# Kernel optimization log

Measured on AMD Instinct MI355X. Metric: run time of the kernel, lower is better.

The kernel has to match this reference:

```python
import jax, jax.numpy as jnp
import numpy as np

D_MSA = 256
D_PAIR = 128
N_HEADS = 8
HEAD_DIM = D_MSA // N_HEADS
EPS = 1e-5


def setup_inputs() -> dict:
    key = jax.random.key(0)
    ks = jax.random.split(key, 14)
    s = 0.02
    return {
        "msa": jax.random.normal(ks[0], (1, 64, 256, D_MSA), dtype=jnp.float32),
        "pair": jax.random.normal(ks[1], (1, 256, 256, D_PAIR), dtype=jnp.float32),
        "Wq": jax.random.normal(ks[2], (D_MSA, D_MSA), dtype=jnp.float32) * s,
        "bq": jnp.zeros((D_MSA,), jnp.float32),
        "Wk": jax.random.normal(ks[3], (D_MSA, D_MSA), dtype=jnp.float32) * s,
        "bk": jnp.zeros((D_MSA,), jnp.float32),
        "Wv": jax.random.normal(ks[4], (D_MSA, D_MSA), dtype=jnp.float32) * s,
        "bv": jnp.zeros((D_MSA,), jnp.float32),
        "Wpb": jax.random.normal(ks[5], (D_PAIR, N_HEADS), dtype=jnp.float32) * s,
        "bpb": jnp.zeros((N_HEADS,), jnp.float32),
        "Wo": jax.random.normal(ks[6], (D_MSA, D_MSA), dtype=jnp.float32) * s,
        "bo": jnp.zeros((D_MSA,), jnp.float32),
        "gamma": jnp.ones((D_MSA,), jnp.float32),
        "beta": jnp.zeros((D_MSA,), jnp.float32),
    }


def reference(msa, pair, Wq, bq, Wk, bk, Wv, bv, Wpb, bpb, Wo, bo, gamma, beta):
    B, N, L, D = msa.shape
    H, Hd = N_HEADS, HEAD_DIM
    # projections -> (B, N, L, H, Hd)
    q = (msa @ Wq + bq).reshape(B, N, L, H, Hd)
    k = (msa @ Wk + bk).reshape(B, N, L, H, Hd)
    v = (msa @ Wv + bv).reshape(B, N, L, H, Hd)
    # scores: (B, N, H, L, L)
    scores = jnp.einsum('bnihd,bnjhd->bnhij', q, k) / jnp.sqrt(jnp.float32(Hd))
    # pair bias: (B, L, L, H) -> (B, H, L, L), broadcast over N
    pb = jnp.transpose(pair @ Wpb + bpb, (0, 3, 1, 2))
    scores = scores + pb[:, None]
    attn = jax.nn.softmax(scores, axis=-1)
    attn_out = jnp.einsum('bnhij,bnjhd->bnihd', attn, v).reshape(B, N, L, D)
    attn_out = attn_out @ Wo + bo
    # residual + LayerNorm
    x = msa + attn_out
    mu = jnp.mean(x, axis=-1, keepdims=True)
    var = jnp.var(x, axis=-1, keepdims=True)
    return (x - mu) * jax.lax.rsqrt(var + EPS) * gamma + beta
```

## Files before the change

### kernel.cpp

```cpp
#include <hip/hip_runtime.h>

#define NSEQ 64
#define LL   256
#define DD   256
#define HH   8
#define HDIM 32

typedef short short8  __attribute__((ext_vector_type(8)));
typedef short short4v __attribute__((ext_vector_type(4)));
typedef float float4v __attribute__((ext_vector_type(4)));

#define MFMA16(a,b,c) __builtin_amdgcn_mfma_f32_16x16x32_bf16((a),(b),(c),0,0,0)

__device__ __forceinline__ float4v zero4() {
  float4v z;
  z[0] = 0.f; z[1] = 0.f; z[2] = 0.f; z[3] = 0.f;
  return z;
}

__device__ __forceinline__ short f2b(float f) {
  unsigned u = __float_as_uint(f);
  u = (u + 0x7fffu + ((u >> 16) & 1u)) >> 16;
  return (short)u;
}

__device__ __forceinline__ float b2f(short s) {
  return __uint_as_float(((unsigned)(unsigned short)s) << 16);
}

__device__ __forceinline__ short8 cvt8(const float* p) {
  float4 a = *(const float4*)p;
  float4 b = *(const float4*)(p + 4);
  short8 r;
  r[0] = f2b(a.x); r[1] = f2b(a.y); r[2] = f2b(a.z); r[3] = f2b(a.w);
  r[4] = f2b(b.x); r[5] = f2b(b.y); r[6] = f2b(b.z); r[7] = f2b(b.w);
  return r;
}

__device__ __forceinline__ void ld_lds16(const void* g, void* l) {
  __builtin_amdgcn_global_load_lds(
      (const __attribute__((address_space(1))) unsigned int*)g,
      (__attribute__((address_space(3))) unsigned int*)l, 16, 0, 0);
}
#define WAIT_VM0() __builtin_amdgcn_s_waitcnt(0x0F70)

#define WT_OFF    0
#define PB_OFF    (4*65536*2)
#define PBF_OFF   (PB_OFF + 8*65536*2)
#define Q_OFF     (PB_OFF + 8*65536*4)
#define K_OFF     (Q_OFF  + 16384*256*2)
#define VT_OFF    (K_OFF  + 16384*256*2)
#define MSA16_OFF (VT_OFF + 16384*256*2)
#define O_OFF     MSA16_OFF

__global__ __launch_bounds__(256) void k1_prep(
    const float* __restrict__ msa,  const float* __restrict__ pair,
    const float* __restrict__ Wq,   const float* __restrict__ Wk,
    const float* __restrict__ Wv,   const float* __restrict__ Wpb,
    const float* __restrict__ bpb,  const float* __restrict__ Wo,
    char* __restrict__ ws)
{
  __shared__ short lds[32 * 264];
  int bx = blockIdx.x, tid = threadIdx.x;
  if (bx < 1024) {
    for (int i = tid; i < 16 * 136; i += 256) lds[i] = 0;
    __syncthreads();
    {
      float4 wv4 = *(const float4*)&Wpb[tid * 4];
      int kk = (tid * 4) >> 3, n0 = (tid * 4) & 7;
      lds[(n0 + 0) * 136 + kk] = f2b(wv4.x);
      lds[(n0 + 1) * 136 + kk] = f2b(wv4.y);
      lds[(n0 + 2) * 136 + kk] = f2b(wv4.z);
      lds[(n0 + 3) * 136 + kk] = f2b(wv4.w);
    }
    __syncthreads();
    int w = tid >> 6, l = tid & 63, q = l >> 4, c = l & 15;
    int base = bx * 64 + w * 16;
    short8 bf[4], af[4];
#pragma unroll
    for (int ks = 0; ks < 4; ks++)
      bf[ks] = *(const short8*)&lds[c * 136 + ks * 32 + q * 8];
#pragma unroll
    for (int ks = 0; ks < 4; ks++)
      af[ks] = cvt8(&pair[(base + c) * 128 + ks * 32 + q * 8]);
    float4v acc = zero4();
#pragma unroll
    for (int ks = 0; ks < 4; ks++) acc = MFMA16(af[ks], bf[ks], acc);
    if (c < 8) {
      float bias = bpb[c];
      int i = bx >> 2, it = i >> 4, lr = i & 15;
      int jt = (bx & 3) * 4 + w;
      short* pbf = (short*)(ws + PBF_OFF);
      int b0 = c * 65536 + it * 4096 + jt * 256 + (lr >> 2) * 64 + (lr & 3) + q * 16;
#pragma unroll
      for (int r = 0; r < 4; r++)
        pbf[b0 + r * 4] = f2b(acc[r] + bias);
    }
  } else if (bx < 1536) {
    int b3 = bx - 1024;
    const float* src = msa + b3 * 8192;
    short* dst = (short*)(ws + MSA16_OFF) + b3 * 8192;
#pragma unroll
    for (int i = 0; i < 8; i++) {
      int idx = i * 1024 + tid * 4;
      float4 v = *(const float4*)&src[idx];
      short4v s;
      s[0] = f2b(v.x); s[1] = f2b(v.y); s[2] = f2b(v.z); s[3] = f2b(v.w);
      *(short4v*)&dst[idx] = s;
    }
  } else {
    int b2 = bx - 1536;
    int mat = b2 >> 3, kt = b2 & 7;
    const float* W = (mat == 0) ? Wq : (mat == 1) ? Wk : (mat == 2) ? Wv : Wo;
    short* wt = (short*)(ws + WT_OFF) + mat * 65536;
#pragma unroll
    for (int i = 0; i < 8; i++) {
      int idx = i * 1024 + tid * 4;
      int k = idx >> 8, n = idx & 255;
      float4 v = *(const float4*)&W[(kt * 32 + k) * 256 + n];
      short4v s;
      s[0] = f2b(v.x); s[1] = f2b(v.y); s[2] = f2b(v.z); s[3] = f2b(v.w);
      *(short4v*)&lds[k * 264 + n] = s;
    }
    __syncthreads();
    int n = tid;
#pragma unroll
    for (int g = 0; g < 4; g++) {
      short8 o;
#pragma unroll
      for (int j = 0; j < 8; j++) o[j] = lds[(g * 8 + j) * 264 + n];
      *(short8*)&wt[n * 256 + kt * 32 + g * 8] = o;
    }
  }
}

__global__ __launch_bounds__(256) void k2_qkv(
    const float* __restrict__ bq, const float* __restrict__ bk,
    const float* __restrict__ bv, char* __restrict__ ws)
{
  __shared__ __align__(16) short lsA[128 * 128];
  __shared__ __align__(16) short lsB[128 * 128];
  int bx = blockIdx.x, tid = threadIdx.x;
  int rt = bx & 127, ct = bx >> 7;
  int m = ct >> 1, cb = (ct & 1) * 128;
  int R0 = rt * 128;
  const short* msa16 = (const short*)(ws + MSA16_OFF);
  const short* wt = (const short*)(ws + WT_OFF) + m * 65536;
  int w = tid >> 6, l = tid & 63, q = l >> 4, c = l & 15;
  int WR = (w & 1) * 64, WC = (w >> 1) * 64;
  float4v acc[4][4];
#pragma unroll
  for (int mt = 0; mt < 4; mt++)
#pragma unroll
    for (int nt = 0; nt < 4; nt++) acc[mt][nt] = zero4();

#pragma unroll 1
  for (int kk = 0; kk < 2; kk++) {
    if (kk) __syncthreads();
#pragma unroll
    for (int i = 0; i < 8; i++) {
      int ci = i * 256 + tid;
      int r = ci >> 4, pos = ci & 15;
      int kc = pos ^ (r & 7);
      ld_lds16(&msa16[(R0 + r) * 256 + kk * 128 + kc * 8], &lsA[ci * 8]);
    }
#pragma unroll
    for (int i = 0; i < 8; i++) {
      int ci = i * 256 + tid;
      int r = ci >> 4, pos = ci & 15;
      int kc = pos ^ (r & 7);
      ld_lds16(&wt[(cb + r) * 256 + kk * 128 + kc * 8], &lsB[ci * 8]);
    }
    WAIT_VM0();
    __syncthreads();
#pragma unroll
    for (int ks = 0; ks < 4; ks++) {
      short8 af[4], bf[4];
#pragma unroll
      for (int mt = 0; mt < 4; mt++) {
        int r = WR + mt * 16 + c;
        int phys = (ks * 4 + q) ^ (r & 7);
        af[mt] = *(const short8*)&lsA[r * 128 + phys * 8];
      }
#pragma unroll
      for (int nt = 0; nt < 4; nt++) {
        int r = WC + nt * 16 + c;
        int phys = (ks * 4 + q) ^ (r & 7);
        bf[nt] = *(const short8*)&lsB[r * 128 + phys * 8];
      }
#pragma unroll
      for (int mt = 0; mt < 4; mt++)
#pragma unroll
        for (int nt = 0; nt < 4; nt++)
          acc[mt][nt] = MFMA16(af[mt], bf[nt], acc[mt][nt]);
    }
  }

  const float* bp = (m == 0) ? bq : (m == 1) ? bk : bv;
  int n = R0 >> 8;
  if (m < 2) {
    short* dst = (short*)(ws + (m == 0 ? Q_OFF : K_OFF));
#pragma unroll
    for (int nt = 0; nt < 4; nt++) {
      int ch = cb + WC + nt * 16 + c;
      float bb = bp[ch];
      int h = ch >> 5, hd = ch & 31;
#pragma unroll
      for (int mt = 0; mt < 4; mt++) {
        int i0 = (R0 & 255) + WR + mt * 16 + q * 4;
#pragma unroll
        for (int r = 0; r < 4; r++)
          dst[((n * HH + h) * 256 + i0 + r) * HDIM + hd] = f2b(acc[mt][nt][r] + bb);
      }
    }
  } else {
    short* vt = (short*)(ws + VT_OFF);
#pragma unroll
    for (int nt = 0; nt < 4; nt++) {
      int ch = cb + WC + nt * 16 + c;
      float bb = bp[ch];
#pragma unroll
      for (int mt = 0; mt < 4; mt++) {
        int j0 = (R0 & 255) + WR + mt * 16 + q * 4;
        short4v s4;
#pragma unroll
        for (int r = 0; r < 4; r++) s4[r] = f2b(acc[mt][nt][r] + bb);
        *(short4v*)&vt[((n * HH + (ch >> 5)) * HDIM + (ch & 31)) * 256 + j0] = s4;
      }
    }
  }
}

__global__ __launch_bounds__(256) void k3_attn(char* __restrict__ ws)
{
  __shared__ short P[4][16 * 136];
  int bx = blockIdx.x, tid = threadIdx.x;
  int qq = bx >> 9, grp = bx & 511;
  int n = grp >> 3, h = grp & 7;
  int w = tid >> 6, l = tid & 63, q = l >> 4, c = l & 15;
  const short* qh = (const short*)(ws + Q_OFF) + (n * HH + h) * 256 * HDIM;
  const short* kh = (const short*)(ws + K_OFF) + (n * HH + h) * 256 * HDIM;
  const short* vt = (const short*)(ws + VT_OFF) + (n * HH + h) * HDIM * 256;
  const short* pbf = (const short*)(ws + PBF_OFF) + (h * 16 + qq * 4 + w) * 4096;
  short* os = (short*)(ws + O_OFF);
  short* Pw = &P[w][0];
  const float scale = 0.17677669529663687f;
  int i0 = qq * 64 + w * 16;
  short8 aq = *(const short8*)&qh[(i0 + c) * HDIM + q * 8];
  float4v o0 = zero4(), o1 = zero4();
  float rs[4] = {0.f, 0.f, 0.f, 0.f};
  float4v s[8];
#pragma unroll 1
  for (int half = 0; half < 2; half++) {
    int jb = half * 8;
#pragma unroll
    for (int jt = 0; jt < 8; jt++) {
      short8 bk8 = *(const short8*)&kh[((jb + jt) * 16 + c) * HDIM + q * 8];
      s[jt] = MFMA16(aq, bk8, zero4());
    }
#pragma unroll
    for (int jt = 0; jt < 8; jt++) {
      short4v pv = *(const short4v*)&pbf[((jb + jt) * 64 + l) * 4];
#pragma unroll
      for (int r = 0; r < 4; r++) {
        float p = __expf(__builtin_fmaf(s[jt][r], scale, b2f(pv[r])));
        s[jt][r] = p;
        rs[r] += p;
      }
    }
#pragma unroll
    for (int jt = 0; jt < 8; jt++)
#pragma unroll
      for (int r = 0; r < 4; r++)
        Pw[(q * 4 + r) * 136 + jt * 16 + c] = f2b(s[jt][r]);
#pragma unroll
    for (int kk = 0; kk < 4; kk++) {
      short8 ap = *(const short8*)&Pw[c * 136 + kk * 32 + q * 8];
      short8 b0 = *(const short8*)&vt[c * 256 + (jb + kk * 2) * 16 + q * 8];
      short8 b1 = *(const short8*)&vt[(16 + c) * 256 + (jb + kk * 2) * 16 + q * 8];
      o0 = MFMA16(ap, b0, o0);
      o1 = MFMA16(ap, b1, o1);
    }
  }
  float inv[4];
#pragma unroll
  for (int r = 0; r < 4; r++) {
    float a = rs[r];
    a += __shfl_xor(a, 1, 64);
    a += __shfl_xor(a, 2, 64);
    a += __shfl_xor(a, 4, 64);
    a += __shfl_xor(a, 8, 64);
    inv[r] = 1.f / a;
  }
#pragma unroll
  for (int r = 0; r < 4; r++) {
    os[(n * 256 + i0 + q * 4 + r) * 256 + h * 32 + c]      = f2b(o0[r] * inv[r]);
    os[(n * 256 + i0 + q * 4 + r) * 256 + h * 32 + 16 + c] = f2b(o1[r] * inv[r]);
  }
}

__global__ __launch_bounds__(256) void k4_out(
    const float* __restrict__ msa, const float* __restrict__ bo,
    const float* __restrict__ gamma, const float* __restrict__ beta,
    const char* __restrict__ ws, float* __restrict__ out)
{
  __shared__ float lnbuf[2][4][16];
  int bx = blockIdx.x, tid = threadIdx.x;
  int w = tid >> 6, l = tid & 63, q = l >> 4, c = l & 15;
  int R0 = bx * 16;
  const short* osrc = (const short*)(ws + O_OFF);
  const short* wto  = (const short*)(ws + WT_OFF) + 3 * 65536;
  short8 af[8];
#pragma unroll
  for (int ks = 0; ks < 8; ks++)
    af[ks] = *(const short8*)&osrc[(R0 + c) * 256 + ks * 32 + q * 8];
  float4v acc[4];
#pragma unroll
  for (int nt = 0; nt < 4; nt++) acc[nt] = zero4();
#pragma unroll
  for (int ks = 0; ks < 8; ks++) {
#pragma unroll
    for (int nt = 0; nt < 4; nt++) {
      short8 bf = *(const short8*)&wto[(w * 64 + nt * 16 + c) * 256 + ks * 32 + q * 8];
      acc[nt] = MFMA16(af[ks], bf, acc[nt]);
    }
  }
  float s1[4] = {0, 0, 0, 0}, s2[4] = {0, 0, 0, 0};
#pragma unroll
  for (int nt = 0; nt < 4; nt++) {
    int col = w * 64 + nt * 16 + c;
    float bb = bo[col];
#pragma unroll
    for (int r = 0; r < 4; r++) {
      float x = acc[nt][r] + bb + msa[(R0 + q * 4 + r) * 256 + col];
      acc[nt][r] = x;
      s1[r] += x;
      s2[r] = __builtin_fmaf(x, x, s2[r]);
    }
  }
#pragma unroll
  for (int r = 0; r < 4; r++) {
    float a = s1[r], b = s2[r];
    a += __shfl_xor(a, 1, 64); b += __shfl_xor(b, 1, 64);
    a += __shfl_xor(a, 2, 64); b += __shfl_xor(b, 2, 64);
    a += __shfl_xor(a, 4, 64); b += __shfl_xor(b, 4, 64);
    a += __shfl_xor(a, 8, 64); b += __shfl_xor(b, 8, 64);
    if (c == 0) {
      lnbuf[0][w][q * 4 + r] = a;
      lnbuf[1][w][q * 4 + r] = b;
    }
  }
  __syncthreads();
  float mu[4], rsd[4];
#pragma unroll
  for (int r = 0; r < 4; r++) {
    int row = q * 4 + r;
    float a = lnbuf[0][0][row] + lnbuf[0][1][row] + lnbuf[0][2][row] + lnbuf[0][3][row];
    float b = lnbuf[1][0][row] + lnbuf[1][1][row] + lnbuf[1][2][row] + lnbuf[1][3][row];
    float m = a * (1.f / 256.f);
    float v = __builtin_fmaf(-m, m, b * (1.f / 256.f));
    mu[r] = m;
    rsd[r] = rsqrtf(v + 1e-5f);
  }
#pragma unroll
  for (int nt = 0; nt < 4; nt++) {
    int col = w * 64 + nt * 16 + c;
    float g = gamma[col], bt = beta[col];
#pragma unroll
    for (int r = 0; r < 4; r++)
      out[(R0 + q * 4 + r) * 256 + col] =
          (acc[nt][r] - mu[r]) * rsd[r] * g + bt;
  }
}

extern "C" void kernel_launch(void* const* d_in, const int* in_sizes, int n_in,
                              void* d_out, int out_size, void* d_ws, size_t ws_size,
                              hipStream_t stream)
{
  const float* msa   = (const float*)d_in[0];
  const float* pair  = (const float*)d_in[1];
  const float* Wq    = (const float*)d_in[2];
  const float* bq    = (const float*)d_in[3];
  const float* Wk    = (const float*)d_in[4];
  const float* bk    = (const float*)d_in[5];
  const float* Wv    = (const float*)d_in[6];
  const float* bv    = (const float*)d_in[7];
  const float* Wpb   = (const float*)d_in[8];
  const float* bpb   = (const float*)d_in[9];
  const float* Wo    = (const float*)d_in[10];
  const float* bo    = (const float*)d_in[11];
  const float* gamma = (const float*)d_in[12];
  const float* beta  = (const float*)d_in[13];
  char* ws = (char*)d_ws;
  float* out = (float*)d_out;

  hipLaunchKernelGGL(k1_prep, dim3(1568), dim3(256), 0, stream,
                     msa, pair, Wq, Wk, Wv, Wpb, bpb, Wo, ws);
  hipLaunchKernelGGL(k2_qkv, dim3(768), dim3(256), 0, stream,
                     bq, bk, bv, ws);
  hipLaunchKernelGGL(k3_attn, dim3(2048), dim3(256), 0, stream, ws);
  hipLaunchKernelGGL(k4_out, dim3(1024), dim3(256), 0, stream,
                     msa, bo, gamma, beta, ws, out);
}
```

Baseline: 181.6 us.

## Move pair-bias projection into QKV kernel and compute full-row softmax first

The pair-bias projection blocks move from the prep kernel into the QKV GEMM launch as extra blocks. The pair read (about 32MB) can then overlap with the QKV GEMM instead of serialising ahead of it, and the prep kernel shrinks to the msa and weight bf16 conversions. In the attention kernel, all 16 score tiles are computed and exponentiated up front, then the P·V passes run. This allows more independent MFMA and exp work to be scheduled together, at the cost of higher register pressure (16 float4 accumulators live at once). The pair-bias blocks in k2 use the larger shared allocation, which may reduce occupancy for those blocks.

```diff
diff --git a/kernel.cpp b/kernel.cpp
--- a/kernel.cpp
+++ b/kernel.cpp
@@ -54,15 +54,61 @@
 #define O_OFF     MSA16_OFF
 
 __global__ __launch_bounds__(256) void k1_prep(
-    const float* __restrict__ msa,  const float* __restrict__ pair,
-    const float* __restrict__ Wq,   const float* __restrict__ Wk,
-    const float* __restrict__ Wv,   const float* __restrict__ Wpb,
-    const float* __restrict__ bpb,  const float* __restrict__ Wo,
-    char* __restrict__ ws)
+    const float* __restrict__ msa, const float* __restrict__ Wq,
+    const float* __restrict__ Wk,  const float* __restrict__ Wv,
+    const float* __restrict__ Wo,  char* __restrict__ ws)
 {
   __shared__ short lds[32 * 264];
   int bx = blockIdx.x, tid = threadIdx.x;
-  if (bx < 1024) {
+  if (bx < 512) {
+    const float* src = msa + bx * 8192;
+    short* dst = (short*)(ws + MSA16_OFF) + bx * 8192;
+#pragma unroll
+    for (int i = 0; i < 8; i++) {
+      int idx = i * 1024 + tid * 4;
+      float4 v = *(const float4*)&src[idx];
+      short4v s;
+      s[0] = f2b(v.x); s[1] = f2b(v.y); s[2] = f2b(v.z); s[3] = f2b(v.w);
+      *(short4v*)&dst[idx] = s;
+    }
+  } else {
+    int b2 = bx - 512;
+    int mat = b2 >> 3, kt = b2 & 7;
+    const float* W = (mat == 0) ? Wq : (mat == 1) ? Wk : (mat == 2) ? Wv : Wo;
+    short* wt = (short*)(ws + WT_OFF) + mat * 65536;
+#pragma unroll
+    for (int i = 0; i < 8; i++) {
+      int idx = i * 1024 + tid * 4;
+      int k = idx >> 8, n = idx & 255;
+      float4 v = *(const float4*)&W[(kt * 32 + k) * 256 + n];
+      short4v s;
+      s[0] = f2b(v.x); s[1] = f2b(v.y); s[2] = f2b(v.z); s[3] = f2b(v.w);
+      *(short4v*)&lds[k * 264 + n] = s;
+    }
+    __syncthreads();
+    int n = tid;
+#pragma unroll
+    for (int g = 0; g < 4; g++) {
+      short8 o;
+#pragma unroll
+      for (int j = 0; j < 8; j++) o[j] = lds[(g * 8 + j) * 264 + n];
+      *(short8*)&wt[n * 256 + kt * 32 + g * 8] = o;
+    }
+  }
+}
+
+__global__ __launch_bounds__(256) void k2_qkv(
+    const float* __restrict__ bq,   const float* __restrict__ bk,
+    const float* __restrict__ bv,   const float* __restrict__ pair,
+    const float* __restrict__ Wpb,  const float* __restrict__ bpb,
+    char* __restrict__ ws)
+{
+  __shared__ __align__(16) short lsA[128 * 128];
+  __shared__ __align__(16) short lsB[128 * 128];
+  int bx = blockIdx.x, tid = threadIdx.x;
+  if (bx >= 768) {
+    int b = bx - 768;
+    short* lds = lsA;
     for (int i = tid; i < 16 * 136; i += 256) lds[i] = 0;
     __syncthreads();
     {
@@ -75,7 +121,7 @@
     }
     __syncthreads();
     int w = tid >> 6, l = tid & 63, q = l >> 4, c = l & 15;
-    int base = bx * 64 + w * 16;
+    int base = b * 64 + w * 16;
     short8 bf[4], af[4];
 #pragma unroll
     for (int ks = 0; ks < 4; ks++)
@@ -88,59 +134,16 @@
     for (int ks = 0; ks < 4; ks++) acc = MFMA16(af[ks], bf[ks], acc);
     if (c < 8) {
       float bias = bpb[c];
-      int i = bx >> 2, it = i >> 4, lr = i & 15;
-      int jt = (bx & 3) * 4 + w;
+      int i = b >> 2, it = i >> 4, lr = i & 15;
+      int jt = (b & 3) * 4 + w;
       short* pbf = (short*)(ws + PBF_OFF);
       int b0 = c * 65536 + it * 4096 + jt * 256 + (lr >> 2) * 64 + (lr & 3) + q * 16;
 #pragma unroll
       for (int r = 0; r < 4; r++)
         pbf[b0 + r * 4] = f2b(acc[r] + bias);
     }
-  } else if (bx < 1536) {
-    int b3 = bx - 1024;
-    const float* src = msa + b3 * 8192;
-    short* dst = (short*)(ws + MSA16_OFF) + b3 * 8192;
-#pragma unroll
-    for (int i = 0; i < 8; i++) {
-      int idx = i * 1024 + tid * 4;
-      float4 v = *(const float4*)&src[idx];
-      short4v s;
-      s[0] = f2b(v.x); s[1] = f2b(v.y); s[2] = f2b(v.z); s[3] = f2b(v.w);
-      *(short4v*)&dst[idx] = s;
-    }
-  } else {
-    int b2 = bx - 1536;
-    int mat = b2 >> 3, kt = b2 & 7;
-    const float* W = (mat == 0) ? Wq : (mat == 1) ? Wk : (mat == 2) ? Wv : Wo;
-    short* wt = (short*)(ws + WT_OFF) + mat * 65536;
-#pragma unroll
-    for (int i = 0; i < 8; i++) {
-      int idx = i * 1024 + tid * 4;
-      int k = idx >> 8, n = idx & 255;
-      float4 v = *(const float4*)&W[(kt * 32 + k) * 256 + n];
-      short4v s;
-      s[0] = f2b(v.x); s[1] = f2b(v.y); s[2] = f2b(v.z); s[3] = f2b(v.w);
-      *(short4v*)&lds[k * 264 + n] = s;
-    }
-    __syncthreads();
-    int n = tid;
-#pragma unroll
-    for (int g = 0; g < 4; g++) {
-      short8 o;
-#pragma unroll
-      for (int j = 0; j < 8; j++) o[j] = lds[(g * 8 + j) * 264 + n];
-      *(short8*)&wt[n * 256 + kt * 32 + g * 8] = o;
-    }
-  }
-}
-
-__global__ __launch_bounds__(256) void k2_qkv(
-    const float* __restrict__ bq, const float* __restrict__ bk,
-    const float* __restrict__ bv, char* __restrict__ ws)
-{
-  __shared__ __align__(16) short lsA[128 * 128];
-  __shared__ __align__(16) short lsB[128 * 128];
-  int bx = blockIdx.x, tid = threadIdx.x;
+    return;
+  }
   int rt = bx & 127, ct = bx >> 7;
   int m = ct >> 1, cb = (ct & 1) * 128;
   int R0 = rt * 128;
@@ -247,39 +250,21 @@
   const float scale = 0.17677669529663687f;
   int i0 = qq * 64 + w * 16;
   short8 aq = *(const short8*)&qh[(i0 + c) * HDIM + q * 8];
-  float4v o0 = zero4(), o1 = zero4();
+  float4v s[16];
+#pragma unroll
+  for (int jt = 0; jt < 16; jt++) {
+    short8 bk8 = *(const short8*)&kh[(jt * 16 + c) * HDIM + q * 8];
+    s[jt] = MFMA16(aq, bk8, zero4());
+  }
   float rs[4] = {0.f, 0.f, 0.f, 0.f};
-  float4v s[8];
-#pragma unroll 1
-  for (int half = 0; half < 2; half++) {
-    int jb = half * 8;
-#pragma unroll
-    for (int jt = 0; jt < 8; jt++) {
-      short8 bk8 = *(const short8*)&kh[((jb + jt) * 16 + c) * HDIM + q * 8];
-      s[jt] = MFMA16(aq, bk8, zero4());
-    }
-#pragma unroll
-    for (int jt = 0; jt < 8; jt++) {
-      short4v pv = *(const short4v*)&pbf[((jb + jt) * 64 + l) * 4];
-#pragma unroll
-      for (int r = 0; r < 4; r++) {
-        float p = __expf(__builtin_fmaf(s[jt][r], scale, b2f(pv[r])));
-        s[jt][r] = p;
-        rs[r] += p;
-      }
-    }
-#pragma unroll
-    for (int jt = 0; jt < 8; jt++)
-#pragma unroll
-      for (int r = 0; r < 4; r++)
-        Pw[(q * 4 + r) * 136 + jt * 16 + c] = f2b(s[jt][r]);
-#pragma unroll
-    for (int kk = 0; kk < 4; kk++) {
-      short8 ap = *(const short8*)&Pw[c * 136 + kk * 32 + q * 8];
-      short8 b0 = *(const short8*)&vt[c * 256 + (jb + kk * 2) * 16 + q * 8];
-      short8 b1 = *(const short8*)&vt[(16 + c) * 256 + (jb + kk * 2) * 16 + q * 8];
-      o0 = MFMA16(ap, b0, o0);
-      o1 = MFMA16(ap, b1, o1);
+#pragma unroll
+  for (int jt = 0; jt < 16; jt++) {
+    short4v pv = *(const short4v*)&pbf[(jt * 64 + l) * 4];
+#pragma unroll
+    for (int r = 0; r < 4; r++) {
+      float p = __expf(__builtin_fmaf(s[jt][r], scale, b2f(pv[r])));
+      s[jt][r] = p;
+      rs[r] += p;
     }
   }
   float inv[4];
@@ -291,6 +276,24 @@
     a += __shfl_xor(a, 4, 64);
     a += __shfl_xor(a, 8, 64);
     inv[r] = 1.f / a;
+  }
+  float4v o0 = zero4(), o1 = zero4();
+#pragma unroll 1
+  for (int half = 0; half < 2; half++) {
+    int jb = half * 8;
+#pragma unroll
+    for (int jt = 0; jt < 8; jt++)
+#pragma unroll
+      for (int r = 0; r < 4; r++)
+        Pw[(q * 4 + r) * 136 + jt * 16 + c] = f2b(s[jb + jt][r]);
+#pragma unroll
+    for (int kk = 0; kk < 4; kk++) {
+      short8 ap = *(const short8*)&Pw[c * 136 + kk * 32 + q * 8];
+      short8 b0 = *(const short8*)&vt[c * 256 + (jb + kk * 2) * 16 + q * 8];
+      short8 b1 = *(const short8*)&vt[(16 + c) * 256 + (jb + kk * 2) * 16 + q * 8];
+      o0 = MFMA16(ap, b0, o0);
+      o1 = MFMA16(ap, b1, o1);
+    }
   }
 #pragma unroll
   for (int r = 0; r < 4; r++) {
@@ -394,10 +397,10 @@
   char* ws = (char*)d_ws;
   float* out = (float*)d_out;
 
-  hipLaunchKernelGGL(k1_prep, dim3(1568), dim3(256), 0, stream,
-                     msa, pair, Wq, Wk, Wv, Wpb, bpb, Wo, ws);
-  hipLaunchKernelGGL(k2_qkv, dim3(768), dim3(256), 0, stream,
-                     bq, bk, bv, ws);
+  hipLaunchKernelGGL(k1_prep, dim3(544), dim3(256), 0, stream,
+                     msa, Wq, Wk, Wv, Wo, ws);
+  hipLaunchKernelGGL(k2_qkv, dim3(1792), dim3(256), 0, stream,
+                     bq, bk, bv, pair, Wpb, bpb, ws);
   hipLaunchKernelGGL(k3_attn, dim3(2048), dim3(256), 0, stream, ws);
   hipLaunchKernelGGL(k4_out, dim3(1024), dim3(256), 0, stream,
                      msa, bo, gamma, beta, ws, out);
```

After: 214.3 us. 1.18x slower.
